# Kernel tuning notes

Measured on AMD Instinct MI355X. Metric: run time of the kernel, lower is better.

The kernel has to match this reference:

```python
import jax, jax.numpy as jnp
import numpy as np

NUM_USERS = 200000
NUM_ITEMS = 100000
NUM_NODES = NUM_USERS + NUM_ITEMS
EMBED_DIM = 64
NUM_EDGES = 2000000
NUM_LAYERS = 2


def setup_inputs() -> dict:
    key = jax.random.key(0)
    k1, k2, k3, k4, k5 = jax.random.split(key, 5)
    u_embs = jax.random.normal(k1, (NUM_USERS, EMBED_DIM), dtype=jnp.float32)
    i_embs = jax.random.normal(k2, (NUM_ITEMS, EMBED_DIM), dtype=jnp.float32)
    edge_src = jax.random.randint(k3, (NUM_EDGES,), 0, NUM_NODES, dtype=jnp.int32)
    edge_dst = jax.random.randint(k4, (NUM_EDGES,), 0, NUM_NODES, dtype=jnp.int32)
    # precomputed symmetric-normalized adjacency weights (1/sqrt(du*di) in the original)
    edge_weight = jax.random.uniform(k5, (NUM_EDGES,), dtype=jnp.float32)
    return {
        "u_embs": u_embs,
        "i_embs": i_embs,
        "edge_src": edge_src,
        "edge_dst": edge_dst,
        "edge_weight": edge_weight,
    }


def _gcn_smooth(embs, edge_src, edge_dst, edge_weight):
    # sparse SpMM: out[d] = sum_{e: dst(e)=d} w_e * embs[src(e)]
    msgs = embs[edge_src] * edge_weight[:, None]  # [E, D]
    return jax.ops.segment_sum(msgs, edge_dst, num_segments=NUM_NODES)


def reference(u_embs, i_embs, edge_src, edge_dst, edge_weight):
    all_embs = jnp.concatenate([u_embs, i_embs], axis=0)  # [N, D]
    acc = all_embs  # running sum over layer outputs (layer 0 included)
    x = all_embs
    for _ in range(NUM_LAYERS):
        x = _gcn_smooth(x, edge_src, edge_dst, edge_weight)
        acc = acc + x
    return acc / jnp.float32(NUM_LAYERS + 1)  # mean over stacked layers
```

## Files before the change

### kernel.cpp

```cpp
#include <hip/hip_runtime.h>
#include <hip/hip_bf16.h>

#define NUSERS 200000
#define NITEMS 100000
#define NNODES 300000
#define EDIM   64
#define NEDGES 2000000
#define SCAN_NB ((NNODES + 255) / 256)
#define FILL_BLOCKS 2048
#define NPASS 4
#define EB4 ((NEDGES / 4 + 255) / 256)
#define CB  ((NNODES * 16 + 255) / 256)
#define SPMM_BLOCKS 2048
#define SPMM_STRIDE (SPMM_BLOCKS * 4)

typedef unsigned short u16;

__device__ __forceinline__ float bf2f(u16 h) {
    return __uint_as_float((unsigned)h << 16);
}
__device__ __forceinline__ u16 f2bf(float f) {
    union { __hip_bfloat16 b; u16 u; } c;
    c.b = __float2bfloat16(f);
    return c.u;
}

__global__ void k_prep(const int4* __restrict__ dst4, int* __restrict__ cnt,
                       const float4* __restrict__ uq, const float4* __restrict__ iq,
                       ushort4* __restrict__ xb4) {
    int b = blockIdx.x;
    if (b < EB4) {
        int i = b * 256 + threadIdx.x;
        if (i < NEDGES / 4) {
            int4 d = dst4[i];
            atomicAdd(&cnt[d.x], 1);
            atomicAdd(&cnt[d.y], 1);
            atomicAdd(&cnt[d.z], 1);
            atomicAdd(&cnt[d.w], 1);
        }
    } else {
        int i = (b - EB4) * 256 + threadIdx.x;
        if (i < NNODES * 16) {
            float4 v = (i < NUSERS * 16) ? uq[i] : iq[i - NUSERS * 16];
            ushort4 h;
            h.x = f2bf(v.x); h.y = f2bf(v.y); h.z = f2bf(v.z); h.w = f2bf(v.w);
            xb4[i] = h;
        }
    }
}


__global__ void k_scan1(int* __restrict__ data, int* __restrict__ bsum) {
    __shared__ int s[256];
    int i = blockIdx.x * 256 + threadIdx.x;
    int v = (i < NNODES) ? data[i] : 0;
    s[threadIdx.x] = v;
    __syncthreads();
    for (int o = 1; o < 256; o <<= 1) {
        int t = (threadIdx.x >= o) ? s[threadIdx.x - o] : 0;
        __syncthreads();
        s[threadIdx.x] += t;
        __syncthreads();
    }
    if (i < NNODES) data[i] = s[threadIdx.x] - v;
    if (threadIdx.x == 255) bsum[blockIdx.x] = s[255];
}

__global__ void k_scan2(int* __restrict__ bsum) {
    __shared__ int s[256];
    __shared__ int carry;
    if (threadIdx.x == 0) carry = 0;
    __syncthreads();
    for (int base = 0; base < SCAN_NB; base += 256) {
        int i = base + threadIdx.x;
        int v = (i < SCAN_NB) ? bsum[i] : 0;
        s[threadIdx.x] = v;
        __syncthreads();
        for (int o = 1; o < 256; o <<= 1) {
            int t = (threadIdx.x >= o) ? s[threadIdx.x - o] : 0;
            __syncthreads();
            s[threadIdx.x] += t;
            __syncthreads();
        }
        if (i < SCAN_NB) bsum[i] = s[threadIdx.x] - v + carry;
        __syncthreads();
        if (threadIdx.x == 0) carry += s[255];
        __syncthreads();
    }
}

__global__ void k_scan3(int* __restrict__ off, const int* __restrict__ bscan,
                        int* __restrict__ wpos) {
    int i = blockIdx.x * 256 + threadIdx.x;
    if (i < NNODES) {
        int v = off[i] + bscan[blockIdx.x];
        off[i] = v;
        wpos[i] = v;
    }
    if (i == 0) off[NNODES] = NEDGES;
}


__global__ void k_fill_win(const int* __restrict__ src, const int4* __restrict__ dst4,
                           const float* __restrict__ w, int* __restrict__ wpos,
                           int2* __restrict__ edata) {
    const int W = (NNODES + NPASS - 1) / NPASS;
    for (int k = 0; k < NPASS; ++k) {
        int lo = k * W;
        int hi = lo + W;
        for (int i = blockIdx.x * 256 + threadIdx.x; i < NEDGES / 4;
             i += FILL_BLOCKS * 256) {
            int4 d = dst4[i];
            int e = i * 4;
            if (d.x >= lo && d.x < hi) {
                int p = atomicAdd(&wpos[d.x], 1);
                edata[p] = make_int2(src[e], __float_as_int(w[e]));
            }
            if (d.y >= lo && d.y < hi) {
                int p = atomicAdd(&wpos[d.y], 1);
                edata[p] = make_int2(src[e + 1], __float_as_int(w[e + 1]));
            }
            if (d.z >= lo && d.z < hi) {
                int p = atomicAdd(&wpos[d.z], 1);
                edata[p] = make_int2(src[e + 2], __float_as_int(w[e + 2]));
            }
            if (d.w >= lo && d.w < hi) {
                int p = atomicAdd(&wpos[d.w], 1);
                edata[p] = make_int2(src[e + 3], __float_as_int(w[e + 3]));
            }
        }
    }
}


__device__ __forceinline__ float4 bfrow(const ushort4* __restrict__ xb4, int s, int l16) {
    const ushort4* p = (const ushort4*)((const char*)xb4 +
                       (((unsigned)s << 7) + ((unsigned)l16 << 3)));
    ushort4 h = *p;
    float4 v;
    v.x = bf2f(h.x); v.y = bf2f(h.y); v.z = bf2f(h.z); v.w = bf2f(h.w);
    return v;
}

__device__ __forceinline__ int2 ld_edge(const int2* __restrict__ e, int i) {
    return *(const int2*)((const char*)e + ((unsigned)i << 3));
}

__global__ __launch_bounds__(256, 8)
void k_spmm1(const ushort4* __restrict__ xb4, const int* __restrict__ off,
             const int2* __restrict__ edata, ushort4* __restrict__ x1b4) {
    const int wid  = threadIdx.x >> 6;
    const int lane = threadIdx.x & 63;
    const int q    = lane >> 4;
    const int l16  = lane & 15;
    int n = blockIdx.x * 4 + wid;
    int o0 = off[n];
    int o1 = off[n + 1];
    while (n < NNODES) {
        int nn = n + SPMM_STRIDE;
        int no0 = 0, no1 = 0;
        if (nn < NNODES) { no0 = off[nn]; no1 = off[nn + 1]; }
        int deg = o1 - o0;
        int cap = o1 - 1; if (cap < 0) cap = 0;
        int b0 = o0 + q;
        int p0 = b0;      if (p0 > cap) p0 = cap;
        int p1 = b0 + 4;  if (p1 > cap) p1 = cap;
        int p2 = b0 + 8;  if (p2 > cap) p2 = cap;
        int p3 = b0 + 12; if (p3 > cap) p3 = cap;
        int2 e0 = ld_edge(edata, p0);
        int2 e1 = ld_edge(edata, p1);
        int2 e2 = ld_edge(edata, p2);
        int2 e3 = ld_edge(edata, p3);
        float4 v0 = make_float4(0.f, 0.f, 0.f, 0.f);
        float4 v1 = v0, v2 = v0, v3 = v0;
        if (q < deg)      v0 = bfrow(xb4, e0.x, l16);
        if (q + 4 < deg)  v1 = bfrow(xb4, e1.x, l16);
        if (q + 8 < deg)  v2 = bfrow(xb4, e2.x, l16);
        if (q + 12 < deg) v3 = bfrow(xb4, e3.x, l16);
        float w0 = __int_as_float(e0.y), w1 = __int_as_float(e1.y);
        float w2 = __int_as_float(e2.y), w3 = __int_as_float(e3.y);
        float4 a0, a1;
        a0.x = w0 * v0.x; a0.y = w0 * v0.y; a0.z = w0 * v0.z; a0.w = w0 * v0.w;
        a1.x = w1 * v1.x; a1.y = w1 * v1.y; a1.z = w1 * v1.z; a1.w = w1 * v1.w;
        a0.x += w2 * v2.x; a0.y += w2 * v2.y; a0.z += w2 * v2.z; a0.w += w2 * v2.w;
        a1.x += w3 * v3.x; a1.y += w3 * v3.y; a1.z += w3 * v3.z; a1.w += w3 * v3.w;
        if (deg > 16) {
            for (int p = b0 + 16; p < o1; p += 4) {
                int2 e = ld_edge(edata, p);
                float4 v = bfrow(xb4, e.x, l16);
                float w = __int_as_float(e.y);
                a0.x += w * v.x; a0.y += w * v.y; a0.z += w * v.z; a0.w += w * v.w;
            }
        }
        a0.x += a1.x; a0.y += a1.y; a0.z += a1.z; a0.w += a1.w;
        a0.x += __shfl_xor(a0.x, 16, 64); a0.y += __shfl_xor(a0.y, 16, 64);
        a0.z += __shfl_xor(a0.z, 16, 64); a0.w += __shfl_xor(a0.w, 16, 64);
        a0.x += __shfl_xor(a0.x, 32, 64); a0.y += __shfl_xor(a0.y, 32, 64);
        a0.z += __shfl_xor(a0.z, 32, 64); a0.w += __shfl_xor(a0.w, 32, 64);
        if (q == 0) {
            ushort4 h;
            h.x = f2bf(a0.x); h.y = f2bf(a0.y); h.z = f2bf(a0.z); h.w = f2bf(a0.w);
            x1b4[(size_t)n * 16 + l16] = h;
        }
        n = nn; o0 = no0; o1 = no1;
    }
}

__global__ __launch_bounds__(256, 8)
void k_spmm2(const float4* __restrict__ uq, const float4* __restrict__ iq,
             const ushort4* __restrict__ x1b4, const int* __restrict__ off,
             const int2* __restrict__ edata, float4* __restrict__ outq) {
    const int wid  = threadIdx.x >> 6;
    const int lane = threadIdx.x & 63;
    const int q    = lane >> 4;
    const int l16  = lane & 15;
    int n = blockIdx.x * 4 + wid;
    int o0 = off[n];
    int o1 = off[n + 1];
    while (n < NNODES) {
        int nn = n + SPMM_STRIDE;
        int no0 = 0, no1 = 0;
        if (nn < NNODES) { no0 = off[nn]; no1 = off[nn + 1]; }
        int deg = o1 - o0;
        int cap = o1 - 1; if (cap < 0) cap = 0;
        int b0 = o0 + q;
        int p0 = b0;      if (p0 > cap) p0 = cap;
        int p1 = b0 + 4;  if (p1 > cap) p1 = cap;
        int p2 = b0 + 8;  if (p2 > cap) p2 = cap;
        int p3 = b0 + 12; if (p3 > cap) p3 = cap;
        int2 e0 = ld_edge(edata, p0);
        int2 e1 = ld_edge(edata, p1);
        int2 e2 = ld_edge(edata, p2);
        int2 e3 = ld_edge(edata, p3);
        float4 v0 = make_float4(0.f, 0.f, 0.f, 0.f);
        float4 v1 = v0, v2 = v0, v3 = v0;
        if (q < deg)      v0 = bfrow(x1b4, e0.x, l16);
        if (q + 4 < deg)  v1 = bfrow(x1b4, e1.x, l16);
        if (q + 8 < deg)  v2 = bfrow(x1b4, e2.x, l16);
        if (q + 12 < deg) v3 = bfrow(x1b4, e3.x, l16);
        float w0 = __int_as_float(e0.y), w1 = __int_as_float(e1.y);
        float w2 = __int_as_float(e2.y), w3 = __int_as_float(e3.y);
        float4 a0, a1;
        a0.x = w0 * v0.x; a0.y = w0 * v0.y; a0.z = w0 * v0.z; a0.w = w0 * v0.w;
        a1.x = w1 * v1.x; a1.y = w1 * v1.y; a1.z = w1 * v1.z; a1.w = w1 * v1.w;
        a0.x += w2 * v2.x; a0.y += w2 * v2.y; a0.z += w2 * v2.z; a0.w += w2 * v2.w;
        a1.x += w3 * v3.x; a1.y += w3 * v3.y; a1.z += w3 * v3.z; a1.w += w3 * v3.w;
        if (deg > 16) {
            for (int p = b0 + 16; p < o1; p += 4) {
                int2 e = ld_edge(edata, p);
                float4 v = bfrow(x1b4, e.x, l16);
                float w = __int_as_float(e.y);
                a0.x += w * v.x; a0.y += w * v.y; a0.z += w * v.z; a0.w += w * v.w;
            }
        }
        a0.x += a1.x; a0.y += a1.y; a0.z += a1.z; a0.w += a1.w;
        a0.x += __shfl_xor(a0.x, 16, 64); a0.y += __shfl_xor(a0.y, 16, 64);
        a0.z += __shfl_xor(a0.z, 16, 64); a0.w += __shfl_xor(a0.w, 16, 64);
        a0.x += __shfl_xor(a0.x, 32, 64); a0.y += __shfl_xor(a0.y, 32, 64);
        a0.z += __shfl_xor(a0.z, 32, 64); a0.w += __shfl_xor(a0.w, 32, 64);
        if (q == 0) {
            size_t ridx = (size_t)n * 16 + l16;
            float4 x0 = (n < NUSERS) ? uq[ridx] : iq[ridx - (size_t)NUSERS * 16];
            float4 x1v = bfrow(x1b4, n, l16);
            const float s = 1.0f / 3.0f;
            float4 r;
            r.x = (x0.x + x1v.x + a0.x) * s;
            r.y = (x0.y + x1v.y + a0.y) * s;
            r.z = (x0.z + x1v.z + a0.z) * s;
            r.w = (x0.w + x1v.w + a0.w) * s;
            outq[ridx] = r;
        }
        n = nn; o0 = no0; o1 = no1;
    }
}


__global__ void scatter_l1(const float* __restrict__ u, const float* __restrict__ it,
                           float* __restrict__ y,
                           const int* __restrict__ src, const int* __restrict__ dst,
                           const float* __restrict__ w) {
    long long t = (long long)blockIdx.x * blockDim.x + threadIdx.x;
    int e = (int)(t >> 4);
    if (e >= NEDGES) return;
    int q = (int)(t & 15);
    int s = src[e], d = dst[e];
    float we = w[e];
    const float* xrow = (s < NUSERS) ? (u + (size_t)s * EDIM)
                                     : (it + (size_t)(s - NUSERS) * EDIM);
    float4 v = ((const float4*)xrow)[q];
    float* yp = y + (size_t)d * EDIM + q * 4;
    atomicAdd(yp + 0, we * v.x);
    atomicAdd(yp + 1, we * v.y);
    atomicAdd(yp + 2, we * v.z);
    atomicAdd(yp + 3, we * v.w);
}

__global__ void scatter_gen(const float* __restrict__ x, float* __restrict__ y,
                            const int* __restrict__ src, const int* __restrict__ dst,
                            const float* __restrict__ w) {
    long long t = (long long)blockIdx.x * blockDim.x + threadIdx.x;
    int e = (int)(t >> 4);
    if (e >= NEDGES) return;
    int q = (int)(t & 15);
    int s = src[e], d = dst[e];
    float we = w[e];
    float4 v = ((const float4*)(x + (size_t)s * EDIM))[q];
    float* yp = y + (size_t)d * EDIM + q * 4;
    atomicAdd(yp + 0, we * v.x);
    atomicAdd(yp + 1, we * v.y);
    atomicAdd(yp + 2, we * v.z);
    atomicAdd(yp + 3, we * v.w);
}

__global__ void final_kernel(const float4* __restrict__ u, const float4* __restrict__ it,
                             const float4* __restrict__ x2, float4* __restrict__ outq) {
    int i = blockIdx.x * blockDim.x + threadIdx.x;
    const int uq = NUSERS * EDIM / 4;
    const int nq = NNODES * EDIM / 4;
    if (i >= nq) return;
    float4 x0 = (i < uq) ? u[i] : it[i - uq];
    float4 x1 = outq[i];
    float4 a  = x2[i];
    const float s = 1.0f / 3.0f;
    float4 r;
    r.x = (x0.x + x1.x + a.x) * s;
    r.y = (x0.y + x1.y + a.y) * s;
    r.z = (x0.z + x1.z + a.z) * s;
    r.w = (x0.w + x1.w + a.w) * s;
    outq[i] = r;
}


extern "C" void kernel_launch(void* const* d_in, const int* in_sizes, int n_in,
                              void* d_out, int out_size, void* d_ws, size_t ws_size,
                              hipStream_t stream) {
    const float* u   = (const float*)d_in[0];
    const float* it  = (const float*)d_in[1];
    const int*   src = (const int*)d_in[2];
    const int*   dst = (const int*)d_in[3];
    const float* w   = (const float*)d_in[4];
    float* out = (float*)d_out;

    const size_t nd = (size_t)NNODES * EDIM;

    int*     off   = (int*)d_ws;
    int*     wpos  = off + NNODES + 8;
    int*     bscan = wpos + NNODES;
    int2*    edata = (int2*)(bscan + 2048);
    ushort4* xb4   = (ushort4*)(edata + NEDGES);
    ushort4* x1b4  = xb4 + (size_t)NNODES * 16;
    const size_t needed =
        (size_t)(NNODES + 8 + NNODES + 2048) * sizeof(int) +
        (size_t)NEDGES * sizeof(int2) +
        (size_t)NNODES * 16 * sizeof(ushort4) * 2;

    dim3 blk(256);

    if (ws_size >= needed) {
        hipMemsetAsync(off, 0, (size_t)NNODES * sizeof(int), stream);
        k_prep <<<EB4 + CB, blk, 0, stream>>>((const int4*)dst, off,
                                              (const float4*)u, (const float4*)it, xb4);
        k_scan1<<<SCAN_NB, blk, 0, stream>>>(off, bscan);
        k_scan2<<<1, blk, 0, stream>>>(bscan);
        k_scan3<<<SCAN_NB, blk, 0, stream>>>(off, bscan, wpos);
        k_fill_win<<<FILL_BLOCKS, blk, 0, stream>>>(src, (const int4*)dst, w, wpos, edata);
        k_spmm1<<<SPMM_BLOCKS, blk, 0, stream>>>(xb4, off, edata, x1b4);
        k_spmm2<<<SPMM_BLOCKS, blk, 0, stream>>>((const float4*)u, (const float4*)it,
                                                 x1b4, off, edata, (float4*)out);
    } else {
        float* A = (float*)d_ws;
        hipMemsetAsync(out, 0, nd * sizeof(float), stream);
        long long nthreads = (long long)NEDGES * 16;
        int sblocks = (int)((nthreads + 255) / 256);
        scatter_l1<<<sblocks, blk, 0, stream>>>(u, it, out, src, dst, w);
        hipMemsetAsync(A, 0, nd * sizeof(float), stream);
        scatter_gen<<<sblocks, blk, 0, stream>>>(out, A, src, dst, w);
        final_kernel<<<(NNODES * EDIM / 4 + 255) / 256, blk, 0, stream>>>(
            (const float4*)u, (const float4*)it, (const float4*)A, (float4*)out);
    }
}
```

Baseline: 515.8 us.

## Software-pipeline edge loads in SpMM and fold scan2 into scan1 via ticket

The SpMM kernels now prefetch the next node's first four edge records and the offsets for the node after that while gathering the current node's rows, so edge-index latency overlaps the row gathers. spmm2 also issues the self-row and input-row loads before the reduction, and the multiply-add chain is reassociated into one accumulator. Separately, the single-block scan2 launch is removed: the last block of scan1 to finish, found through an atomic ticket, scans the block sums, saving one kernel launch. The prefetching raises register pressure under launch_bounds(256,8), and the ticket scheme depends on the threadfence ordering being correct.

```diff
diff --git a/kernel.cpp b/kernel.cpp
--- a/kernel.cpp
+++ b/kernel.cpp
@@ -27,8 +27,9 @@
 
 __global__ void k_prep(const int4* __restrict__ dst4, int* __restrict__ cnt,
                        const float4* __restrict__ uq, const float4* __restrict__ iq,
-                       ushort4* __restrict__ xb4) {
+                       ushort4* __restrict__ xb4, int* __restrict__ ticket) {
     int b = blockIdx.x;
+    if (b == 0 && threadIdx.x == 0) *ticket = 0;
     if (b < EB4) {
         int i = b * 256 + threadIdx.x;
         if (i < NEDGES / 4) {
@@ -50,8 +51,10 @@
 }
 
 
-__global__ void k_scan1(int* __restrict__ data, int* __restrict__ bsum) {
+__global__ void k_scan1(int* __restrict__ data, int* __restrict__ bsum,
+                        int* __restrict__ ticket) {
     __shared__ int s[256];
+    __shared__ int lastblk;
     int i = blockIdx.x * 256 + threadIdx.x;
     int v = (i < NNODES) ? data[i] : 0;
     s[threadIdx.x] = v;
@@ -64,28 +67,31 @@
     }
     if (i < NNODES) data[i] = s[threadIdx.x] - v;
     if (threadIdx.x == 255) bsum[blockIdx.x] = s[255];
-}
-
-__global__ void k_scan2(int* __restrict__ bsum) {
-    __shared__ int s[256];
-    __shared__ int carry;
-    if (threadIdx.x == 0) carry = 0;
+    __threadfence();
+    if (threadIdx.x == 0)
+        lastblk = (atomicAdd(ticket, 1) == SCAN_NB - 1);
     __syncthreads();
-    for (int base = 0; base < SCAN_NB; base += 256) {
-        int i = base + threadIdx.x;
-        int v = (i < SCAN_NB) ? bsum[i] : 0;
-        s[threadIdx.x] = v;
+    if (lastblk) {
+        __threadfence();
+        __shared__ int carry;
+        if (threadIdx.x == 0) carry = 0;
         __syncthreads();
-        for (int o = 1; o < 256; o <<= 1) {
-            int t = (threadIdx.x >= o) ? s[threadIdx.x - o] : 0;
+        for (int base = 0; base < SCAN_NB; base += 256) {
+            int j = base + threadIdx.x;
+            int bv = (j < SCAN_NB) ? bsum[j] : 0;
+            s[threadIdx.x] = bv;
             __syncthreads();
-            s[threadIdx.x] += t;
+            for (int o = 1; o < 256; o <<= 1) {
+                int t = (threadIdx.x >= o) ? s[threadIdx.x - o] : 0;
+                __syncthreads();
+                s[threadIdx.x] += t;
+                __syncthreads();
+            }
+            if (j < SCAN_NB) bsum[j] = s[threadIdx.x] - bv + carry;
             __syncthreads();
-        }
-        if (i < SCAN_NB) bsum[i] = s[threadIdx.x] - v + carry;
-        __syncthreads();
-        if (threadIdx.x == 0) carry += s[255];
-        __syncthreads();
+            if (threadIdx.x == 0) carry += s[255];
+            __syncthreads();
+        }
     }
 }
 
@@ -154,55 +160,62 @@
     const int q    = lane >> 4;
     const int l16  = lane & 15;
     int n = blockIdx.x * 4 + wid;
-    int o0 = off[n];
-    int o1 = off[n + 1];
+    int oc0 = off[n], oc1 = off[n + 1];
+    int degC = oc1 - oc0;
+    int capC = oc1 - 1; if (capC < 0) capC = 0;
+    int bC = oc0 + q;
+    int2 eC0 = ld_edge(edata, min(bC,      capC));
+    int2 eC1 = ld_edge(edata, min(bC + 4,  capC));
+    int2 eC2 = ld_edge(edata, min(bC + 8,  capC));
+    int2 eC3 = ld_edge(edata, min(bC + 12, capC));
+    int nN = n + SPMM_STRIDE;
+    int on0 = 0, on1 = 0;
+    if (nN < NNODES) { on0 = off[nN]; on1 = off[nN + 1]; }
     while (n < NNODES) {
-        int nn = n + SPMM_STRIDE;
-        int no0 = 0, no1 = 0;
-        if (nn < NNODES) { no0 = off[nn]; no1 = off[nn + 1]; }
-        int deg = o1 - o0;
-        int cap = o1 - 1; if (cap < 0) cap = 0;
-        int b0 = o0 + q;
-        int p0 = b0;      if (p0 > cap) p0 = cap;
-        int p1 = b0 + 4;  if (p1 > cap) p1 = cap;
-        int p2 = b0 + 8;  if (p2 > cap) p2 = cap;
-        int p3 = b0 + 12; if (p3 > cap) p3 = cap;
-        int2 e0 = ld_edge(edata, p0);
-        int2 e1 = ld_edge(edata, p1);
-        int2 e2 = ld_edge(edata, p2);
-        int2 e3 = ld_edge(edata, p3);
-        float4 v0 = make_float4(0.f, 0.f, 0.f, 0.f);
-        float4 v1 = v0, v2 = v0, v3 = v0;
-        if (q < deg)      v0 = bfrow(xb4, e0.x, l16);
-        if (q + 4 < deg)  v1 = bfrow(xb4, e1.x, l16);
-        if (q + 8 < deg)  v2 = bfrow(xb4, e2.x, l16);
-        if (q + 12 < deg) v3 = bfrow(xb4, e3.x, l16);
-        float w0 = __int_as_float(e0.y), w1 = __int_as_float(e1.y);
-        float w2 = __int_as_float(e2.y), w3 = __int_as_float(e3.y);
-        float4 a0, a1;
-        a0.x = w0 * v0.x; a0.y = w0 * v0.y; a0.z = w0 * v0.z; a0.w = w0 * v0.w;
-        a1.x = w1 * v1.x; a1.y = w1 * v1.y; a1.z = w1 * v1.z; a1.w = w1 * v1.w;
-        a0.x += w2 * v2.x; a0.y += w2 * v2.y; a0.z += w2 * v2.z; a0.w += w2 * v2.w;
-        a1.x += w3 * v3.x; a1.y += w3 * v3.y; a1.z += w3 * v3.z; a1.w += w3 * v3.w;
-        if (deg > 16) {
-            for (int p = b0 + 16; p < o1; p += 4) {
+        float4 z = make_float4(0.f, 0.f, 0.f, 0.f);
+        float4 v0 = z, v1 = z, v2 = z, v3 = z;
+        if (q < degC)      v0 = bfrow(xb4, eC0.x, l16);
+        if (q + 4 < degC)  v1 = bfrow(xb4, eC1.x, l16);
+        if (q + 8 < degC)  v2 = bfrow(xb4, eC2.x, l16);
+        if (q + 12 < degC) v3 = bfrow(xb4, eC3.x, l16);
+        int degN = on1 - on0;
+        int capN = on1 - 1; if (capN < 0) capN = 0;
+        int bN = on0 + q;
+        int2 eN0 = ld_edge(edata, min(bN,      capN));
+        int2 eN1 = ld_edge(edata, min(bN + 4,  capN));
+        int2 eN2 = ld_edge(edata, min(bN + 8,  capN));
+        int2 eN3 = ld_edge(edata, min(bN + 12, capN));
+        int nNN = nN + SPMM_STRIDE;
+        int onn0 = 0, onn1 = 0;
+        if (nNN < NNODES) { onn0 = off[nNN]; onn1 = off[nNN + 1]; }
+        float w0 = __int_as_float(eC0.y), w1 = __int_as_float(eC1.y);
+        float w2 = __int_as_float(eC2.y), w3 = __int_as_float(eC3.y);
+        float4 a;
+        a.x = w0*v0.x + w1*v1.x + w2*v2.x + w3*v3.x;
+        a.y = w0*v0.y + w1*v1.y + w2*v2.y + w3*v3.y;
+        a.z = w0*v0.z + w1*v1.z + w2*v2.z + w3*v3.z;
+        a.w = w0*v0.w + w1*v1.w + w2*v2.w + w3*v3.w;
+        if (degC > 16) {
+            for (int p = bC + 16; p < oc1; p += 4) {
                 int2 e = ld_edge(edata, p);
                 float4 v = bfrow(xb4, e.x, l16);
                 float w = __int_as_float(e.y);
-                a0.x += w * v.x; a0.y += w * v.y; a0.z += w * v.z; a0.w += w * v.w;
-            }
-        }
-        a0.x += a1.x; a0.y += a1.y; a0.z += a1.z; a0.w += a1.w;
-        a0.x += __shfl_xor(a0.x, 16, 64); a0.y += __shfl_xor(a0.y, 16, 64);
-        a0.z += __shfl_xor(a0.z, 16, 64); a0.w += __shfl_xor(a0.w, 16, 64);
-        a0.x += __shfl_xor(a0.x, 32, 64); a0.y += __shfl_xor(a0.y, 32, 64);
-        a0.z += __shfl_xor(a0.z, 32, 64); a0.w += __shfl_xor(a0.w, 32, 64);
+                a.x += w*v.x; a.y += w*v.y; a.z += w*v.z; a.w += w*v.w;
+            }
+        }
+        a.x += __shfl_xor(a.x, 16, 64); a.y += __shfl_xor(a.y, 16, 64);
+        a.z += __shfl_xor(a.z, 16, 64); a.w += __shfl_xor(a.w, 16, 64);
+        a.x += __shfl_xor(a.x, 32, 64); a.y += __shfl_xor(a.y, 32, 64);
+        a.z += __shfl_xor(a.z, 32, 64); a.w += __shfl_xor(a.w, 32, 64);
         if (q == 0) {
             ushort4 h;
-            h.x = f2bf(a0.x); h.y = f2bf(a0.y); h.z = f2bf(a0.z); h.w = f2bf(a0.w);
+            h.x = f2bf(a.x); h.y = f2bf(a.y); h.z = f2bf(a.z); h.w = f2bf(a.w);
             x1b4[(size_t)n * 16 + l16] = h;
         }
-        n = nn; o0 = no0; o1 = no1;
+        n = nN; nN = nNN;
+        oc1 = on1; on0 = onn0; on1 = onn1;
+        degC = degN; capC = capN; bC = bN;
+        eC0 = eN0; eC1 = eN1; eC2 = eN2; eC3 = eN3;
     }
 }
 
@@ -215,62 +228,69 @@
     const int q    = lane >> 4;
     const int l16  = lane & 15;
     int n = blockIdx.x * 4 + wid;
-    int o0 = off[n];
-    int o1 = off[n + 1];
+    int oc0 = off[n], oc1 = off[n + 1];
+    int degC = oc1 - oc0;
+    int capC = oc1 - 1; if (capC < 0) capC = 0;
+    int bC = oc0 + q;
+    int2 eC0 = ld_edge(edata, min(bC,      capC));
+    int2 eC1 = ld_edge(edata, min(bC + 4,  capC));
+    int2 eC2 = ld_edge(edata, min(bC + 8,  capC));
+    int2 eC3 = ld_edge(edata, min(bC + 12, capC));
+    int nN = n + SPMM_STRIDE;
+    int on0 = 0, on1 = 0;
+    if (nN < NNODES) { on0 = off[nN]; on1 = off[nN + 1]; }
     while (n < NNODES) {
-        int nn = n + SPMM_STRIDE;
-        int no0 = 0, no1 = 0;
-        if (nn < NNODES) { no0 = off[nn]; no1 = off[nn + 1]; }
-        int deg = o1 - o0;
-        int cap = o1 - 1; if (cap < 0) cap = 0;
-        int b0 = o0 + q;
-        int p0 = b0;      if (p0 > cap) p0 = cap;
-        int p1 = b0 + 4;  if (p1 > cap) p1 = cap;
-        int p2 = b0 + 8;  if (p2 > cap) p2 = cap;
-        int p3 = b0 + 12; if (p3 > cap) p3 = cap;
-        int2 e0 = ld_edge(edata, p0);
-        int2 e1 = ld_edge(edata, p1);
-        int2 e2 = ld_edge(edata, p2);
-        int2 e3 = ld_edge(edata, p3);
-        float4 v0 = make_float4(0.f, 0.f, 0.f, 0.f);
-        float4 v1 = v0, v2 = v0, v3 = v0;
-        if (q < deg)      v0 = bfrow(x1b4, e0.x, l16);
-        if (q + 4 < deg)  v1 = bfrow(x1b4, e1.x, l16);
-        if (q + 8 < deg)  v2 = bfrow(x1b4, e2.x, l16);
-        if (q + 12 < deg) v3 = bfrow(x1b4, e3.x, l16);
-        float w0 = __int_as_float(e0.y), w1 = __int_as_float(e1.y);
-        float w2 = __int_as_float(e2.y), w3 = __int_as_float(e3.y);
-        float4 a0, a1;
-        a0.x = w0 * v0.x; a0.y = w0 * v0.y; a0.z = w0 * v0.z; a0.w = w0 * v0.w;
-        a1.x = w1 * v1.x; a1.y = w1 * v1.y; a1.z = w1 * v1.z; a1.w = w1 * v1.w;
-        a0.x += w2 * v2.x; a0.y += w2 * v2.y; a0.z += w2 * v2.z; a0.w += w2 * v2.w;
-        a1.x += w3 * v3.x; a1.y += w3 * v3.y; a1.z += w3 * v3.z; a1.w += w3 * v3.w;
-        if (deg > 16) {
-            for (int p = b0 + 16; p < o1; p += 4) {
+        float4 z = make_float4(0.f, 0.f, 0.f, 0.f);
+        float4 v0 = z, v1 = z, v2 = z, v3 = z;
+        if (q < degC)      v0 = bfrow(x1b4, eC0.x, l16);
+        if (q + 4 < degC)  v1 = bfrow(x1b4, eC1.x, l16);
+        if (q + 8 < degC)  v2 = bfrow(x1b4, eC2.x, l16);
+        if (q + 12 < degC) v3 = bfrow(x1b4, eC3.x, l16);
+        int degN = on1 - on0;
+        int capN = on1 - 1; if (capN < 0) capN = 0;
+        int bN = on0 + q;
+        int2 eN0 = ld_edge(edata, min(bN,      capN));
+        int2 eN1 = ld_edge(edata, min(bN + 4,  capN));
+        int2 eN2 = ld_edge(edata, min(bN + 8,  capN));
+        int2 eN3 = ld_edge(edata, min(bN + 12, capN));
+        int nNN = nN + SPMM_STRIDE;
+        int onn0 = 0, onn1 = 0;
+        if (nNN < NNODES) { onn0 = off[nNN]; onn1 = off[nNN + 1]; }
+        size_t ridx = (size_t)n * 16 + l16;
+        float4 x0 = (n < NUSERS) ? uq[ridx] : iq[ridx - (size_t)NUSERS * 16];
+        float4 x1s = bfrow(x1b4, n, l16);
+        float w0 = __int_as_float(eC0.y), w1 = __int_as_float(eC1.y);
+        float w2 = __int_as_float(eC2.y), w3 = __int_as_float(eC3.y);
+        float4 a;
+        a.x = w0*v0.x + w1*v1.x + w2*v2.x + w3*v3.x;
+        a.y = w0*v0.y + w1*v1.y + w2*v2.y + w3*v3.y;
+        a.z = w0*v0.z + w1*v1.z + w2*v2.z + w3*v3.z;
+        a.w = w0*v0.w + w1*v1.w + w2*v2.w + w3*v3.w;
+        if (degC > 16) {
+            for (int p = bC + 16; p < oc1; p += 4) {
                 int2 e = ld_edge(edata, p);
                 float4 v = bfrow(x1b4, e.x, l16);
                 float w = __int_as_float(e.y);
-                a0.x += w * v.x; a0.y += w * v.y; a0.z += w * v.z; a0.w += w * v.w;
-            }
-        }
-        a0.x += a1.x; a0.y += a1.y; a0.z += a1.z; a0.w += a1.w;
-        a0.x += __shfl_xor(a0.x, 16, 64); a0.y += __shfl_xor(a0.y, 16, 64);
-        a0.z += __shfl_xor(a0.z, 16, 64); a0.w += __shfl_xor(a0.w, 16, 64);
-        a0.x += __shfl_xor(a0.x, 32, 64); a0.y += __shfl_xor(a0.y, 32, 64);
-        a0.z += __shfl_xor(a0.z, 32, 64); a0.w += __shfl_xor(a0.w, 32, 64);
+                a.x += w*v.x; a.y += w*v.y; a.z += w*v.z; a.w += w*v.w;
+            }
+        }
+        a.x += __shfl_xor(a.x, 16, 64); a.y += __shfl_xor(a.y, 16, 64);
+        a.z += __shfl_xor(a.z, 16, 64); a.w += __shfl_xor(a.w, 16, 64);
+        a.x += __shfl_xor(a.x, 32, 64); a.y += __shfl_xor(a.y, 32, 64);
+        a.z += __shfl_xor(a.z, 32, 64); a.w += __shfl_xor(a.w, 32, 64);
         if (q == 0) {
-            size_t ridx = (size_t)n * 16 + l16;
-            float4 x0 = (n < NUSERS) ? uq[ridx] : iq[ridx - (size_t)NUSERS * 16];
-            float4 x1v = bfrow(x1b4, n, l16);
             const float s = 1.0f / 3.0f;
             float4 r;
-            r.x = (x0.x + x1v.x + a0.x) * s;
-            r.y = (x0.y + x1v.y + a0.y) * s;
-            r.z = (x0.z + x1v.z + a0.z) * s;
-            r.w = (x0.w + x1v.w + a0.w) * s;
+            r.x = (x0.x + x1s.x + a.x) * s;
+            r.y = (x0.y + x1s.y + a.y) * s;
+            r.z = (x0.z + x1s.z + a.z) * s;
+            r.w = (x0.w + x1s.w + a.w) * s;
             outq[ridx] = r;
         }
-        n = nn; o0 = no0; o1 = no1;
+        n = nN; nN = nNN;
+        oc1 = on1; on0 = onn0; on1 = onn1;
+        degC = degN; capC = capN; bC = bN;
+        eC0 = eN0; eC1 = eN1; eC2 = eN2; eC3 = eN3;
     }
 }
 
@@ -349,6 +369,7 @@
     int2*    edata = (int2*)(bscan + 2048);
     ushort4* xb4   = (ushort4*)(edata + NEDGES);
     ushort4* x1b4  = xb4 + (size_t)NNODES * 16;
+    int*     ticket = bscan + 2047;
     const size_t needed =
         (size_t)(NNODES + 8 + NNODES + 2048) * sizeof(int) +
         (size_t)NEDGES * sizeof(int2) +
@@ -359,9 +380,9 @@
     if (ws_size >= needed) {
         hipMemsetAsync(off, 0, (size_t)NNODES * sizeof(int), stream);
         k_prep <<<EB4 + CB, blk, 0, stream>>>((const int4*)dst, off,
-                                              (const float4*)u, (const float4*)it, xb4);
-        k_scan1<<<SCAN_NB, blk, 0, stream>>>(off, bscan);
-        k_scan2<<<1, blk, 0, stream>>>(bscan);
+                                              (const float4*)u, (const float4*)it,
+                                              xb4, ticket);
+        k_scan1<<<SCAN_NB, blk, 0, stream>>>(off, bscan, ticket);
         k_scan3<<<SCAN_NB, blk, 0, stream>>>(off, bscan, wpos);
         k_fill_win<<<FILL_BLOCKS, blk, 0, stream>>>(src, (const int4*)dst, w, wpos, edata);
         k_spmm1<<<SPMM_BLOCKS, blk, 0, stream>>>(xb4, off, edata, x1b4);
```

Measured after the change: 587.9 us. 1.14x slower.
